# Performance work log

Hardware: AMD Instinct MI355X
Metric: run time of the kernel (lower is better)

Reference implementation:

```python
import jax, jax.numpy as jnp
import numpy as np

B, S, D, H = 2, 2048, 1024, 16
HD = D // H  # 64


def setup_inputs() -> dict:
    key = jax.random.key(0)
    ks = jax.random.split(key, 7)
    scale = 1.0 / np.sqrt(D)
    return {
        "embeddings": jax.random.normal(ks[0], (B, S, D), dtype=jnp.float32),
        "W_kv": jax.random.uniform(ks[1], (D, 2 * D), jnp.float32, -scale, scale),
        "b_kv": jax.random.uniform(ks[2], (2 * D,), jnp.float32, -scale, scale),
        "W_q": jax.random.uniform(ks[3], (D, D), jnp.float32, -scale, scale),
        "b_q": jax.random.uniform(ks[4], (D,), jnp.float32, -scale, scale),
        "W_o": jax.random.uniform(ks[5], (D, D), jnp.float32, -scale, scale),
        "b_o": jax.random.uniform(ks[6], (D,), jnp.float32, -scale, scale),
    }


def reference(embeddings, W_kv, b_kv, W_q, b_q, W_o, b_o):
    # kv projection -> [B, S, H, 2*HD] -> [B, H, S, 2*HD]
    kv = (embeddings @ W_kv + b_kv).reshape(B, S, H, 2 * HD).transpose(0, 2, 1, 3)
    q = (embeddings @ W_q + b_q).reshape(B, S, H, HD).transpose(0, 2, 1, 3)
    k, v = kv[..., :HD], kv[..., HD:]
    # naive scaled dot-product attention (full [B,H,S,S] score matrix)
    scores = jnp.einsum("bhqd,bhkd->bhqk", q, k) / jnp.sqrt(jnp.float32(HD))
    attn = jax.nn.softmax(scores, axis=-1)
    ctx = jnp.einsum("bhqk,bhkd->bhqd", attn, v)  # [B,H,S,HD]
    ctx = ctx.transpose(0, 2, 1, 3).reshape(B, S, D)
    return ctx @ W_o + b_o
```

## Files before the change

### kernel.cpp

```cpp
#include <hip/hip_runtime.h>
#include <hip/hip_bf16.h>


typedef unsigned short ushort;
typedef __attribute__((ext_vector_type(4))) float f32x4;
typedef __attribute__((ext_vector_type(16))) float f32x16;
typedef __attribute__((ext_vector_type(8))) __bf16 bf16x8;
typedef __attribute__((ext_vector_type(8))) unsigned short u16x8;
typedef __attribute__((ext_vector_type(4))) unsigned short u16x4;
typedef __attribute__((ext_vector_type(4))) unsigned int u32x4;

#define LOG2E 1.44269504088896340736f

constexpr int Bc = 2, Sc = 2048, Dc = 1024, Hc = 16, HDc = 64;

__device__ inline ushort f2bf(float f) {
    unsigned u = __builtin_bit_cast(unsigned, f);
    u += 0x7fffu + ((u >> 16) & 1u);
    return (ushort)(u >> 16);
}

__device__ inline float fexp2(float x) {
#if __has_builtin(__builtin_amdgcn_exp2f)
    return __builtin_amdgcn_exp2f(x);
#else
    return exp2f(x);
#endif
}

__device__ inline void gload16(const void* g, void* l) {
    __builtin_amdgcn_global_load_lds((const __attribute__((address_space(1))) void*)g,
                                     (__attribute__((address_space(3))) void*)l, 16, 0, 0);
}

__device__ inline f32x4 mfma16(bf16x8 a, bf16x8 b, f32x4 c) {
    return __builtin_amdgcn_mfma_f32_16x16x32_bf16(a, b, c, 0, 0, 0);
}
__device__ inline f32x16 mfma32(bf16x8 a, bf16x8 b, f32x16 c) {
    return __builtin_amdgcn_mfma_f32_32x32x16_bf16(a, b, c, 0, 0, 0);
}
__device__ inline unsigned cvtpk(float lo, float hi_) {
    unsigned r; asm("v_cvt_pk_bf16_f32 %0, %1, %2" : "=v"(r) : "v"(lo), "v"(hi_)); return r;
}
__device__ inline void swap32(unsigned& a, unsigned& b) {
    asm("v_permlane32_swap_b32 %0, %1" : "+v"(a), "+v"(b));
}

__global__ __launch_bounds__(256) void prep_k(const float* __restrict__ emb,
                                              ushort* __restrict__ embb,
                                              const float* __restrict__ Wkv,
                                              const float* __restrict__ Wq,
                                              const float* __restrict__ Wo,
                                              ushort* __restrict__ WtAll) {
    const int bid = blockIdx.x;
    if (bid < 2048) {
        int i = bid * 256 + threadIdx.x;
        const float4* p = (const float4*)emb;
        float4 a = p[2 * i], b = p[2 * i + 1];
        u16x8 r;
        r[0] = f2bf(a.x); r[1] = f2bf(a.y); r[2] = f2bf(a.z); r[3] = f2bf(a.w);
        r[4] = f2bf(b.x); r[5] = f2bf(b.y); r[6] = f2bf(b.z); r[7] = f2bf(b.w);
        ((u16x8*)embb)[i] = r;
        return;
    }
    __shared__ float t[32][33];
    int tb = bid - 2048;
    const float* W; int N, rowofs;
    if (tb < 2048)      { W = Wkv; N = 2048; rowofs = 0; }
    else if (tb < 3072) { W = Wq;  N = 1024; rowofs = 2048; tb -= 2048; }
    else                { W = Wo;  N = 1024; rowofs = 3072; tb -= 3072; }
    const int nbx = N >> 5;
    const int bx = tb % nbx, by = tb / nbx;
    const int tx = threadIdx.x & 31, ty = threadIdx.x >> 5;
    const int bj = bx * 32, bi = by * 32;
#pragma unroll
    for (int i = 0; i < 4; i++) {
        int r = ty + i * 8;
        t[r][tx] = W[(size_t)(bi + r) * N + bj + tx];
    }
    __syncthreads();
#pragma unroll
    for (int i = 0; i < 4; i++) {
        int r = ty + i * 8;
        WtAll[(size_t)(rowofs + bj + r) * 1024 + bi + tx] = f2bf(t[tx][r]);
    }
}

template <int MODE>
__global__ __launch_bounds__(256) void gemm_bt_k(const ushort* __restrict__ A,
                                                 const ushort* __restrict__ Bt,
                                                 const float* __restrict__ bias,
                                                 const float* __restrict__ bias2,
                                                 void* __restrict__ Cout,
                                                 ushort* __restrict__ Vout,
                                                 ushort* __restrict__ Qout,
                                                 int M, int N, int K) {
    __shared__ __align__(16) char sA[2][8192];
    __shared__ __align__(16) char sB[2][8192];
    const int tid = threadIdx.x;
    const int nbc = N >> 7;
    const int cpx = (gridDim.x >> 3);
    const int swzb = (blockIdx.x & 7) * cpx + (blockIdx.x >> 3);
    const int brow = swzb / nbc, bcol = swzb % nbc;
    const int w = tid >> 6, lane = tid & 63;
    const int wr = w >> 1, wc = w & 1;
    const int lg = lane >> 4, l16 = lane & 15;

    f32x4 acc[4][4] = {};

    const int r0 = tid >> 2;
    const int sl = (tid & 3) ^ (r0 & 3);
    const ushort* a0 = A + (size_t)(brow * 128 + r0) * K + sl * 8;
    const ushort* a1 = A + (size_t)(brow * 128 + 64 + r0) * K + sl * 8;
    const ushort* b0 = Bt + (size_t)(bcol * 128 + r0) * K + sl * 8;
    const ushort* b1 = Bt + (size_t)(bcol * 128 + 64 + r0) * K + sl * 8;

    const int arow = wr * 64 + l16;
    const int bcolr = wc * 64 + l16;

    auto STAGE = [&](int buf, int k0) {
        gload16(a0 + k0, sA[buf] + w * 1024);
        gload16(a1 + k0, sA[buf] + 4096 + w * 1024);
        gload16(b0 + k0, sB[buf] + w * 1024);
        gload16(b1 + k0, sB[buf] + 4096 + w * 1024);
    };

    const int nk = K >> 5;
    STAGE(0, 0);

    for (int k0 = 0; k0 < nk; k0++) {
        const int buf = k0 & 1;
        if (k0 < nk - 1) {
            STAGE(buf ^ 1, (k0 + 1) << 5);
            asm volatile("s_waitcnt vmcnt(4)" ::: "memory");
        } else {
            asm volatile("s_waitcnt vmcnt(0)" ::: "memory");
        }
        __builtin_amdgcn_s_barrier();
        __builtin_amdgcn_sched_barrier(0);

        bf16x8 af[4], bfr[4];
#pragma unroll
        for (int rf = 0; rf < 4; rf++) {
            int rr = arow + rf * 16;
            af[rf] = *(const bf16x8*)(sA[buf] + rr * 64 + ((lg * 16) ^ ((rr & 3) << 4)));
        }
#pragma unroll
        for (int cf = 0; cf < 4; cf++) {
            int rr = bcolr + cf * 16;
            bfr[cf] = *(const bf16x8*)(sB[buf] + rr * 64 + ((lg * 16) ^ ((rr & 3) << 4)));
        }
#pragma unroll
        for (int rf = 0; rf < 4; rf++)
#pragma unroll
            for (int cf = 0; cf < 4; cf++)
                acc[rf][cf] = mfma16(af[rf], bfr[cf], acc[rf][cf]);
        __builtin_amdgcn_s_barrier();
    }

#pragma unroll
    for (int cf = 0; cf < 4; cf++) {
        const int col = bcol * 128 + wc * 64 + cf * 16 + l16;
        if constexpr (MODE == 3) {
            if (col < 2048) {
                const float bv = bias[col];
                const int h = col >> 7, lo = col & 127;
#pragma unroll
                for (int rf = 0; rf < 4; rf++) {
                    int row = brow * 128 + wr * 64 + rf * 16 + lg * 4;
                    int b = row >> 11, s = row & 2047;
                    if (lo < 64) {
                        ushort* Kout = (ushort*)Cout;
#pragma unroll
                        for (int r = 0; r < 4; r++)
                            Kout[((size_t)(b * 16 + h) * 2048 + s + r) * 64 + lo] =
                                f2bf(acc[rf][cf][r] + bv);
                    } else {
                        u16x4 pk;
#pragma unroll
                        for (int r = 0; r < 4; r++) pk[r] = f2bf(acc[rf][cf][r] + bv);
                        *(u16x4*)(Vout + ((size_t)(b * 16 + h) * 64 + (lo - 64)) * 2048 + s) = pk;
                    }
                }
            } else {
                const int qc = col - 2048;
                const float bv = bias2[qc];
                const float qs = 0.125f * LOG2E;
#pragma unroll
                for (int rf = 0; rf < 4; rf++) {
                    int row = brow * 128 + wr * 64 + rf * 16 + lg * 4;
#pragma unroll
                    for (int r = 0; r < 4; r++)
                        Qout[(size_t)(row + r) * 1024 + qc] =
                            f2bf((acc[rf][cf][r] + bv) * qs);
                }
            }
        } else {
            const float bv = bias[col];
#pragma unroll
            for (int rf = 0; rf < 4; rf++) {
                int row = brow * 128 + wr * 64 + rf * 16 + lg * 4;
#pragma unroll
                for (int r = 0; r < 4; r++) {
                    float v = acc[rf][cf][r] + bv;
                    if (MODE == 1) ((float*)Cout)[(size_t)(row + r) * N + col] = v;
                    else           ((ushort*)Cout)[(size_t)(row + r) * N + col] = f2bf(v);
                }
            }
        }
    }
}

__global__ __launch_bounds__(256, 2) void attn3_k(const ushort* __restrict__ Qg,
                                                  const ushort* __restrict__ Kg,
                                                  const ushort* __restrict__ Vg,
                                                  ushort* __restrict__ ctx) {
    __shared__ __align__(16) char sK[2][16384];
    __shared__ __align__(16) char sV[2][16384];
    __shared__ float lx2[256];
    const int tid = threadIdx.x;
    const int wg = ((blockIdx.x & 7) << 6) | (blockIdx.x >> 3);
    const int bh = wg >> 4, qt = wg & 15;
    const int b = bh >> 4, h = bh & 15;
    const int w = tid >> 6, lane = tid & 63;
    const int ql = lane & 31, hi = lane >> 5;
    const int ksub = w & 1;
    const int qq = w >> 1;

    const ushort* Kh = Kg + (size_t)bh * (Sc * 64);
    const ushort* Vh = Vg + (size_t)bh * (64 * Sc);

    const int qrow0 = qt * 128 + qq * 64 + ql;
    bf16x8 qf[2][4];
#pragma unroll
    for (int qg = 0; qg < 2; qg++) {
        const ushort* qp = Qg + ((size_t)(b * Sc + qrow0 + qg * 32)) * Dc + h * HDc + hi * 8;
#pragma unroll
        for (int jd = 0; jd < 4; jd++) qf[qg][jd] = *(const bf16x8*)(qp + jd * 16);
    }

    const u16x8 ones_u = {0x3F80, 0x3F80, 0x3F80, 0x3F80, 0x3F80, 0x3F80, 0x3F80, 0x3F80};
    const bf16x8 ones8 = __builtin_bit_cast(bf16x8, ones_u);

    const int l8 = lane >> 3;
    const int sl = (lane & 7) ^ l8;

    f32x16 o[2][2] = {};
    f32x16 ls[2] = {};
    const float MH = 8.0f * LOG2E;
    const int sw = (ql & 7) << 4;

    auto STAGE = [&](int buf, int kt) {
#pragma unroll
        for (int j = 0; j < 4; j++) {
            gload16(Kh + (size_t)(kt * 128 + w * 32 + j * 8 + l8) * 64 + sl * 8,
                    sK[buf] + w * 4096 + j * 1024);
            gload16(Vh + (size_t)((w & 1) * 32 + j * 8 + l8) * Sc +
                        kt * 128 + (w >> 1) * 64 + sl * 8,
                    sV[buf] + (w >> 1) * 8192 + (w & 1) * 4096 + j * 1024);
        }
    };

    int cur = 0;
    STAGE(0, 0);

    constexpr int NT = Sc / 128;
    for (int kt = 0; kt < NT; kt++) {
        if (kt < NT - 1) {
            STAGE(cur ^ 1, kt + 1);
            asm volatile("s_waitcnt vmcnt(8)" ::: "memory");
        } else {
            asm volatile("s_waitcnt vmcnt(0)" ::: "memory");
        }
        __builtin_amdgcn_s_barrier();
        __builtin_amdgcn_sched_barrier(0);

#pragma unroll
        for (int kh = 0; kh < 2; kh++) {
            bf16x8 kf[4];
            {
                const char* kb = sK[cur] + (kh * 64 + ksub * 32 + ql) * 128;
#pragma unroll
                for (int jd = 0; jd < 4; jd++)
                    kf[jd] = *(const bf16x8*)(kb + ((jd * 32 + hi * 16) ^ sw));
            }

            f32x16 st[2];
#pragma unroll
            for (int qg = 0; qg < 2; qg++)
#pragma unroll
                for (int i = 0; i < 16; i++) st[qg][i] = -MH;
            __builtin_amdgcn_s_setprio(1);
#pragma unroll
            for (int qg = 0; qg < 2; qg++)
#pragma unroll
                for (int jd = 0; jd < 4; jd++)
                    st[qg] = mfma32(kf[jd], qf[qg][jd], st[qg]);
            __builtin_amdgcn_s_setprio(0);

#pragma unroll
            for (int qg = 0; qg < 2; qg++)
#pragma unroll
                for (int i = 0; i < 16; i++) st[qg][i] = fexp2(st[qg][i]);

            bf16x8 pf[2][2];
#pragma unroll
            for (int qg = 0; qg < 2; qg++) {
                unsigned a0 = cvtpk(st[qg][0],  st[qg][1]);
                unsigned a1 = cvtpk(st[qg][2],  st[qg][3]);
                unsigned a2 = cvtpk(st[qg][4],  st[qg][5]);
                unsigned a3 = cvtpk(st[qg][6],  st[qg][7]);
                swap32(a0, a2); swap32(a1, a3);
                u32x4 f0v = {a0, a1, a2, a3};
                pf[qg][0] = __builtin_bit_cast(bf16x8, f0v);
                unsigned c0 = cvtpk(st[qg][8],  st[qg][9]);
                unsigned c1 = cvtpk(st[qg][10], st[qg][11]);
                unsigned c2 = cvtpk(st[qg][12], st[qg][13]);
                unsigned c3 = cvtpk(st[qg][14], st[qg][15]);
                swap32(c0, c2); swap32(c1, c3);
                u32x4 f1v = {c0, c1, c2, c3};
                pf[qg][1] = __builtin_bit_cast(bf16x8, f1v);
            }

            bf16x8 vf[2][2];
#pragma unroll
            for (int dg = 0; dg < 2; dg++) {
                const char* vb = sV[cur] + kh * 8192 + (dg * 32 + ql) * 128;
#pragma unroll
                for (int ks = 0; ks < 2; ks++)
                    vf[dg][ks] = *(const bf16x8*)(vb + ((ksub * 64 + ks * 32 + hi * 16) ^ sw));
            }

            __builtin_amdgcn_s_setprio(1);
#pragma unroll
            for (int qg = 0; qg < 2; qg++)
#pragma unroll
                for (int ks = 0; ks < 2; ks++) {
                    o[0][qg] = mfma32(vf[0][ks], pf[qg][ks], o[0][qg]);
                    o[1][qg] = mfma32(vf[1][ks], pf[qg][ks], o[1][qg]);
                    ls[qg]   = mfma32(ones8,     pf[qg][ks], ls[qg]);
                }
            __builtin_amdgcn_s_setprio(0);
        }

        __builtin_amdgcn_s_barrier();
        cur ^= 1;
    }

    __syncthreads();
    float* ox = qq ? (float*)sV : (float*)sK;
    if (ksub) {
#pragma unroll
        for (int dg = 0; dg < 2; dg++)
#pragma unroll
            for (int qg = 0; qg < 2; qg++)
#pragma unroll
                for (int i = 0; i < 16; i++)
                    ox[((dg * 2 + qg) * 16 + i) * 64 + lane] = o[dg][qg][i];
        lx2[(qq * 2 + 0) * 64 + lane] = ls[0][0];
        lx2[(qq * 2 + 1) * 64 + lane] = ls[1][0];
    }
    __syncthreads();
    if (!ksub) {
#pragma unroll
        for (int dg = 0; dg < 2; dg++)
#pragma unroll
            for (int qg = 0; qg < 2; qg++)
#pragma unroll
                for (int i = 0; i < 16; i++)
                    o[dg][qg][i] += ox[((dg * 2 + qg) * 16 + i) * 64 + lane];
        const float inv0 = 1.0f / (ls[0][0] + lx2[(qq * 2 + 0) * 64 + lane]);
        const float inv1 = 1.0f / (ls[1][0] + lx2[(qq * 2 + 1) * 64 + lane]);
#pragma unroll
        for (int qg = 0; qg < 2; qg++) {
            const float inv = qg ? inv1 : inv0;
            ushort* cp = ctx + ((size_t)(b * Sc + qrow0 + qg * 32)) * Dc + h * HDc;
#pragma unroll
            for (int dg = 0; dg < 2; dg++)
#pragma unroll
                for (int g = 0; g < 4; g++) {
                    u16x4 pk;
#pragma unroll
                    for (int r = 0; r < 4; r++)
                        pk[r] = f2bf(o[dg][qg][g * 4 + r] * inv);
                    *(u16x4*)(cp + dg * 32 + g * 8 + hi * 4) = pk;
                }
        }
    }
}

extern "C" void kernel_launch(void* const* d_in, const int* in_sizes, int n_in,
                              void* d_out, int out_size, void* d_ws, size_t ws_size,
                              hipStream_t stream) {
    const float* emb  = (const float*)d_in[0];
    const float* W_kv = (const float*)d_in[1];
    const float* b_kv = (const float*)d_in[2];
    const float* W_q  = (const float*)d_in[3];
    const float* b_q  = (const float*)d_in[4];
    const float* W_o  = (const float*)d_in[5];
    const float* b_o  = (const float*)d_in[6];
    float* out = (float*)d_out;

    const int BS = Bc * Sc;
    ushort* embb  = (ushort*)d_ws;
    ushort* wallt = embb  + (size_t)BS * Dc;
    ushort* wot   = wallt + (size_t)3 * Dc * Dc;
    ushort* Kb    = wallt + (size_t)4 * Dc * Dc;
    ushort* Vtb   = Kb    + (size_t)32 * Sc * HDc;
    ushort* Qb    = Vtb   + (size_t)32 * Sc * HDc;
    ushort* ctxb  = Qb    + (size_t)BS * Dc;

    prep_k<<<6144, 256, 0, stream>>>(emb, embb, W_kv, W_q, W_o, wallt);

    gemm_bt_k<3><<<(BS / 128) * (3072 / 128), 256, 0, stream>>>(
        embb, wallt, b_kv, b_q, Kb, Vtb, Qb, BS, 3072, Dc);

    attn3_k<<<Bc * Hc * (Sc / 128), 256, 0, stream>>>(Qb, Kb, Vtb, ctxb);

    gemm_bt_k<1><<<(BS / 128) * (Dc / 128), 256, 0, stream>>>(
        ctxb, wot, b_o, nullptr, out, nullptr, nullptr, BS, Dc, Dc);
}
```

Before: 113.6 us.

## Split attention keys across four waves with private LDS tiles, drop barriers

The attention kernel now processes 64 query rows per block instead of 128, and all four waves share those queries while each handles its own 32-key slice of every 128-key tile. Each wave stages its own K/V slice into a private double-buffered LDS region, so the per-tile workgroup barriers are removed and waves only wait on their own loads. Partial outputs and row sums from three waves are reduced through LDS into wave 0 at the end, and the grid doubles to 1024 blocks. In exchange, each block reloads the full K/V for half as many queries, doubling global K/V traffic, and the final cross-wave reduction is larger.

```diff
diff --git a/kernel.cpp b/kernel.cpp
--- a/kernel.cpp
+++ b/kernel.cpp
@@ -211,58 +211,56 @@
     }
 }
 
-__global__ __launch_bounds__(256, 2) void attn3_k(const ushort* __restrict__ Qg,
+__global__ __launch_bounds__(256, 2) void attn4_k(const ushort* __restrict__ Qg,
                                                   const ushort* __restrict__ Kg,
                                                   const ushort* __restrict__ Vg,
                                                   ushort* __restrict__ ctx) {
-    __shared__ __align__(16) char sK[2][16384];
-    __shared__ __align__(16) char sV[2][16384];
-    __shared__ float lx2[256];
+    __shared__ __align__(16) char sS[4][2][8192];
+    __shared__ float lxa[3 * 128];
     const int tid = threadIdx.x;
-    const int wg = ((blockIdx.x & 7) << 6) | (blockIdx.x >> 3);
-    const int bh = wg >> 4, qt = wg & 15;
+    const int wg = ((blockIdx.x & 7) << 7) | (blockIdx.x >> 3);
+    const int bh = wg >> 5, qt = wg & 31;
     const int b = bh >> 4, h = bh & 15;
     const int w = tid >> 6, lane = tid & 63;
     const int ql = lane & 31, hi = lane >> 5;
-    const int ksub = w & 1;
-    const int qq = w >> 1;
 
     const ushort* Kh = Kg + (size_t)bh * (Sc * 64);
     const ushort* Vh = Vg + (size_t)bh * (64 * Sc);
 
-    const int qrow0 = qt * 128 + qq * 64 + ql;
+    const int l8 = lane >> 3;
+    const int kch = (lane & 7) ^ l8;
+    const int vhalf = (lane & 7) >> 2;
+    const int vkk = (lane & 3) ^ (l8 & 3);
+
+    auto STAGE = [&](int buf, int kt) {
+        const int kkb = kt * 128 + w * 32;
+#pragma unroll
+        for (int j = 0; j < 4; j++) {
+            gload16(Kh + (size_t)(kkb + j * 8 + l8) * 64 + kch * 8,
+                    sS[w][buf] + j * 1024);
+            gload16(Vh + (size_t)(j * 8 + l8 + vhalf * 32) * Sc + kkb + vkk * 8,
+                    sS[w][buf] + 4096 + j * 1024);
+        }
+    };
+
+    int cur = 0;
+    STAGE(0, 0);
+
+    const int q0 = qt * 64;
     bf16x8 qf[2][4];
 #pragma unroll
     for (int qg = 0; qg < 2; qg++) {
-        const ushort* qp = Qg + ((size_t)(b * Sc + qrow0 + qg * 32)) * Dc + h * HDc + hi * 8;
+        const ushort* qp = Qg + ((size_t)(b * Sc + q0 + qg * 32 + ql)) * Dc + h * HDc + hi * 8;
 #pragma unroll
         for (int jd = 0; jd < 4; jd++) qf[qg][jd] = *(const bf16x8*)(qp + jd * 16);
     }
 
     const u16x8 ones_u = {0x3F80, 0x3F80, 0x3F80, 0x3F80, 0x3F80, 0x3F80, 0x3F80, 0x3F80};
     const bf16x8 ones8 = __builtin_bit_cast(bf16x8, ones_u);
-
-    const int l8 = lane >> 3;
-    const int sl = (lane & 7) ^ l8;
 
     f32x16 o[2][2] = {};
     f32x16 ls[2] = {};
     const float MH = 8.0f * LOG2E;
-    const int sw = (ql & 7) << 4;
-
-    auto STAGE = [&](int buf, int kt) {
-#pragma unroll
-        for (int j = 0; j < 4; j++) {
-            gload16(Kh + (size_t)(kt * 128 + w * 32 + j * 8 + l8) * 64 + sl * 8,
-                    sK[buf] + w * 4096 + j * 1024);
-            gload16(Vh + (size_t)((w & 1) * 32 + j * 8 + l8) * Sc +
-                        kt * 128 + (w >> 1) * 64 + sl * 8,
-                    sV[buf] + (w >> 1) * 8192 + (w & 1) * 4096 + j * 1024);
-        }
-    };
-
-    int cur = 0;
-    STAGE(0, 0);
 
     constexpr int NT = Sc / 128;
     for (int kt = 0; kt < NT; kt++) {
@@ -272,109 +270,109 @@
         } else {
             asm volatile("s_waitcnt vmcnt(0)" ::: "memory");
         }
-        __builtin_amdgcn_s_barrier();
         __builtin_amdgcn_sched_barrier(0);
 
-#pragma unroll
-        for (int kh = 0; kh < 2; kh++) {
-            bf16x8 kf[4];
-            {
-                const char* kb = sK[cur] + (kh * 64 + ksub * 32 + ql) * 128;
-#pragma unroll
-                for (int jd = 0; jd < 4; jd++)
-                    kf[jd] = *(const bf16x8*)(kb + ((jd * 32 + hi * 16) ^ sw));
+        const char* kb = sS[w][cur];
+        const char* vb = sS[w][cur] + 4096;
+
+        bf16x8 kf[4];
+#pragma unroll
+        for (int jd = 0; jd < 4; jd++)
+            kf[jd] = *(const bf16x8*)(kb + ql * 128 + ((((jd << 1) | hi) ^ (ql & 7)) << 4));
+
+        f32x16 st[2];
+#pragma unroll
+        for (int qg = 0; qg < 2; qg++)
+#pragma unroll
+            for (int i = 0; i < 16; i++) st[qg][i] = -MH;
+        __builtin_amdgcn_s_setprio(1);
+#pragma unroll
+        for (int qg = 0; qg < 2; qg++)
+#pragma unroll
+            for (int jd = 0; jd < 4; jd++)
+                st[qg] = mfma32(kf[jd], qf[qg][jd], st[qg]);
+        __builtin_amdgcn_s_setprio(0);
+
+#pragma unroll
+        for (int qg = 0; qg < 2; qg++)
+#pragma unroll
+            for (int i = 0; i < 16; i++) st[qg][i] = fexp2(st[qg][i]);
+
+        bf16x8 pf[2][2];
+#pragma unroll
+        for (int qg = 0; qg < 2; qg++) {
+            unsigned a0 = cvtpk(st[qg][0],  st[qg][1]);
+            unsigned a1 = cvtpk(st[qg][2],  st[qg][3]);
+            unsigned a2 = cvtpk(st[qg][4],  st[qg][5]);
+            unsigned a3 = cvtpk(st[qg][6],  st[qg][7]);
+            swap32(a0, a2); swap32(a1, a3);
+            u32x4 f0v = {a0, a1, a2, a3};
+            pf[qg][0] = __builtin_bit_cast(bf16x8, f0v);
+            unsigned c0 = cvtpk(st[qg][8],  st[qg][9]);
+            unsigned c1 = cvtpk(st[qg][10], st[qg][11]);
+            unsigned c2 = cvtpk(st[qg][12], st[qg][13]);
+            unsigned c3 = cvtpk(st[qg][14], st[qg][15]);
+            swap32(c0, c2); swap32(c1, c3);
+            u32x4 f1v = {c0, c1, c2, c3};
+            pf[qg][1] = __builtin_bit_cast(bf16x8, f1v);
+        }
+
+        bf16x8 vf[2][2];
+#pragma unroll
+        for (int dg = 0; dg < 2; dg++)
+#pragma unroll
+            for (int ks = 0; ks < 2; ks++)
+                vf[dg][ks] = *(const bf16x8*)(vb + ql * 128 + dg * 64 +
+                                              ((((ks << 1) | hi) ^ (ql & 3)) << 4));
+
+        __builtin_amdgcn_s_setprio(1);
+#pragma unroll
+        for (int qg = 0; qg < 2; qg++)
+#pragma unroll
+            for (int ks = 0; ks < 2; ks++) {
+                o[0][qg] = mfma32(vf[0][ks], pf[qg][ks], o[0][qg]);
+                o[1][qg] = mfma32(vf[1][ks], pf[qg][ks], o[1][qg]);
+                ls[qg]   = mfma32(ones8,     pf[qg][ks], ls[qg]);
             }
-
-            f32x16 st[2];
+        __builtin_amdgcn_s_setprio(0);
+
+        cur ^= 1;
+    }
+
+    __syncthreads();
+    float* ox = (float*)sS;
+    if (w) {
+        const int base = (w - 1) * 4096;
+#pragma unroll
+        for (int dg = 0; dg < 2; dg++)
 #pragma unroll
             for (int qg = 0; qg < 2; qg++)
 #pragma unroll
-                for (int i = 0; i < 16; i++) st[qg][i] = -MH;
-            __builtin_amdgcn_s_setprio(1);
-#pragma unroll
-            for (int qg = 0; qg < 2; qg++)
-#pragma unroll
-                for (int jd = 0; jd < 4; jd++)
-                    st[qg] = mfma32(kf[jd], qf[qg][jd], st[qg]);
-            __builtin_amdgcn_s_setprio(0);
-
-#pragma unroll
-            for (int qg = 0; qg < 2; qg++)
-#pragma unroll
-                for (int i = 0; i < 16; i++) st[qg][i] = fexp2(st[qg][i]);
-
-            bf16x8 pf[2][2];
-#pragma unroll
-            for (int qg = 0; qg < 2; qg++) {
-                unsigned a0 = cvtpk(st[qg][0],  st[qg][1]);
-                unsigned a1 = cvtpk(st[qg][2],  st[qg][3]);
-                unsigned a2 = cvtpk(st[qg][4],  st[qg][5]);
-                unsigned a3 = cvtpk(st[qg][6],  st[qg][7]);
-                swap32(a0, a2); swap32(a1, a3);
-                u32x4 f0v = {a0, a1, a2, a3};
-                pf[qg][0] = __builtin_bit_cast(bf16x8, f0v);
-                unsigned c0 = cvtpk(st[qg][8],  st[qg][9]);
-                unsigned c1 = cvtpk(st[qg][10], st[qg][11]);
-                unsigned c2 = cvtpk(st[qg][12], st[qg][13]);
-                unsigned c3 = cvtpk(st[qg][14], st[qg][15]);
-                swap32(c0, c2); swap32(c1, c3);
-                u32x4 f1v = {c0, c1, c2, c3};
-                pf[qg][1] = __builtin_bit_cast(bf16x8, f1v);
-            }
-
-            bf16x8 vf[2][2];
-#pragma unroll
-            for (int dg = 0; dg < 2; dg++) {
-                const char* vb = sV[cur] + kh * 8192 + (dg * 32 + ql) * 128;
-#pragma unroll
-                for (int ks = 0; ks < 2; ks++)
-                    vf[dg][ks] = *(const bf16x8*)(vb + ((ksub * 64 + ks * 32 + hi * 16) ^ sw));
-            }
-
-            __builtin_amdgcn_s_setprio(1);
-#pragma unroll
-            for (int qg = 0; qg < 2; qg++)
-#pragma unroll
-                for (int ks = 0; ks < 2; ks++) {
-                    o[0][qg] = mfma32(vf[0][ks], pf[qg][ks], o[0][qg]);
-                    o[1][qg] = mfma32(vf[1][ks], pf[qg][ks], o[1][qg]);
-                    ls[qg]   = mfma32(ones8,     pf[qg][ks], ls[qg]);
-                }
-            __builtin_amdgcn_s_setprio(0);
-        }
-
-        __builtin_amdgcn_s_barrier();
-        cur ^= 1;
-    }
-
+                for (int i = 0; i < 16; i++)
+                    ox[base + ((dg * 2 + qg) * 16 + i) * 64 + lane] = o[dg][qg][i];
+        lxa[(w - 1) * 128 + 0 * 64 + lane] = ls[0][0];
+        lxa[(w - 1) * 128 + 1 * 64 + lane] = ls[1][0];
+    }
     __syncthreads();
-    float* ox = qq ? (float*)sV : (float*)sK;
-    if (ksub) {
-#pragma unroll
-        for (int dg = 0; dg < 2; dg++)
-#pragma unroll
-            for (int qg = 0; qg < 2; qg++)
-#pragma unroll
-                for (int i = 0; i < 16; i++)
-                    ox[((dg * 2 + qg) * 16 + i) * 64 + lane] = o[dg][qg][i];
-        lx2[(qq * 2 + 0) * 64 + lane] = ls[0][0];
-        lx2[(qq * 2 + 1) * 64 + lane] = ls[1][0];
-    }
-    __syncthreads();
-    if (!ksub) {
-#pragma unroll
-        for (int dg = 0; dg < 2; dg++)
-#pragma unroll
-            for (int qg = 0; qg < 2; qg++)
-#pragma unroll
-                for (int i = 0; i < 16; i++)
-                    o[dg][qg][i] += ox[((dg * 2 + qg) * 16 + i) * 64 + lane];
-        const float inv0 = 1.0f / (ls[0][0] + lx2[(qq * 2 + 0) * 64 + lane]);
-        const float inv1 = 1.0f / (ls[1][0] + lx2[(qq * 2 + 1) * 64 + lane]);
+    if (w == 0) {
+        float l_run[2] = {ls[0][0], ls[1][0]};
+#pragma unroll
+        for (int wv = 0; wv < 3; wv++) {
+            const int base = wv * 4096;
+#pragma unroll
+            for (int dg = 0; dg < 2; dg++)
+#pragma unroll
+                for (int qg = 0; qg < 2; qg++)
+#pragma unroll
+                    for (int i = 0; i < 16; i++)
+                        o[dg][qg][i] += ox[base + ((dg * 2 + qg) * 16 + i) * 64 + lane];
+            l_run[0] += lxa[wv * 128 + 0 * 64 + lane];
+            l_run[1] += lxa[wv * 128 + 1 * 64 + lane];
+        }
 #pragma unroll
         for (int qg = 0; qg < 2; qg++) {
-            const float inv = qg ? inv1 : inv0;
-            ushort* cp = ctx + ((size_t)(b * Sc + qrow0 + qg * 32)) * Dc + h * HDc;
+            const float inv = 1.0f / l_run[qg];
+            ushort* cp = ctx + ((size_t)(b * Sc + q0 + qg * 32 + ql)) * Dc + h * HDc;
 #pragma unroll
             for (int dg = 0; dg < 2; dg++)
 #pragma unroll
@@ -415,7 +413,7 @@
     gemm_bt_k<3><<<(BS / 128) * (3072 / 128), 256, 0, stream>>>(
         embb, wallt, b_kv, b_q, Kb, Vtb, Qb, BS, 3072, Dc);
 
-    attn3_k<<<Bc * Hc * (Sc / 128), 256, 0, stream>>>(Qb, Kb, Vtb, ctxb);
+    attn4_k<<<Bc * Hc * (Sc / 64), 256, 0, stream>>>(Qb, Kb, Vtb, ctxb);
 
     gemm_bt_k<1><<<(BS / 128) * (Dc / 128), 256, 0, stream>>>(
         ctxb, wot, b_o, nullptr, out, nullptr, nullptr, BS, Dc, Dc);
```

Result: slower. 119.6 us (+5.3%).

## Software-pipeline QK^T, exp, and PV across key sub-tiles in attention loop

Applied to the files above, without the earlier changes.

Restructures the inner attention loop so that the exponentiation and PV MFMAs of the previous key sub-tile are interleaved with the QK^T MFMAs of the next sub-tile. The second half's scores and V fragments are carried in registers across iterations. A zero-initialised prologue (exp2(-128) scores times zero V) and an epilogue handle the edges. This lets transcendental ALU work overlap matrix-core work, at the cost of more live registers (extra f32x16 scores and V fragments), which may lower occupancy or cause spills.

```diff
diff --git a/kernel.cpp b/kernel.cpp
--- a/kernel.cpp
+++ b/kernel.cpp
@@ -250,6 +250,52 @@
     const float MH = 8.0f * LOG2E;
     const int sw = (ql & 7) << 4;
 
+    f32x16 stp[2];
+    bf16x8 vfp[2][2];
+#pragma unroll
+    for (int qg = 0; qg < 2; qg++)
+#pragma unroll
+        for (int i = 0; i < 16; i++) stp[qg][i] = -128.0f;
+    {
+        const u16x8 z = {0, 0, 0, 0, 0, 0, 0, 0};
+#pragma unroll
+        for (int dg = 0; dg < 2; dg++)
+#pragma unroll
+            for (int ks = 0; ks < 2; ks++) vfp[dg][ks] = __builtin_bit_cast(bf16x8, z);
+    }
+
+    auto PACK = [&](f32x16 (&s)[2], bf16x8 (&p)[2][2]) {
+#pragma unroll
+        for (int qg = 0; qg < 2; qg++) {
+            unsigned a0 = cvtpk(s[qg][0],  s[qg][1]);
+            unsigned a1 = cvtpk(s[qg][2],  s[qg][3]);
+            unsigned a2 = cvtpk(s[qg][4],  s[qg][5]);
+            unsigned a3 = cvtpk(s[qg][6],  s[qg][7]);
+            swap32(a0, a2); swap32(a1, a3);
+            u32x4 f0v = {a0, a1, a2, a3};
+            p[qg][0] = __builtin_bit_cast(bf16x8, f0v);
+            unsigned c0 = cvtpk(s[qg][8],  s[qg][9]);
+            unsigned c1 = cvtpk(s[qg][10], s[qg][11]);
+            unsigned c2 = cvtpk(s[qg][12], s[qg][13]);
+            unsigned c3 = cvtpk(s[qg][14], s[qg][15]);
+            swap32(c0, c2); swap32(c1, c3);
+            u32x4 f1v = {c0, c1, c2, c3};
+            p[qg][1] = __builtin_bit_cast(bf16x8, f1v);
+        }
+    };
+    auto PV = [&](bf16x8 (&v)[2][2], bf16x8 (&p)[2][2]) {
+        __builtin_amdgcn_s_setprio(1);
+#pragma unroll
+        for (int qg = 0; qg < 2; qg++)
+#pragma unroll
+            for (int ks = 0; ks < 2; ks++) {
+                o[0][qg] = mfma32(v[0][ks], p[qg][ks], o[0][qg]);
+                o[1][qg] = mfma32(v[1][ks], p[qg][ks], o[1][qg]);
+                ls[qg]   = mfma32(ones8,    p[qg][ks], ls[qg]);
+            }
+        __builtin_amdgcn_s_setprio(0);
+    };
+
     auto STAGE = [&](int buf, int kt) {
 #pragma unroll
         for (int j = 0; j < 4; j++) {
@@ -275,76 +321,95 @@
         __builtin_amdgcn_s_barrier();
         __builtin_amdgcn_sched_barrier(0);
 
-#pragma unroll
-        for (int kh = 0; kh < 2; kh++) {
-            bf16x8 kf[4];
-            {
-                const char* kb = sK[cur] + (kh * 64 + ksub * 32 + ql) * 128;
-#pragma unroll
-                for (int jd = 0; jd < 4; jd++)
-                    kf[jd] = *(const bf16x8*)(kb + ((jd * 32 + hi * 16) ^ sw));
-            }
-
-            f32x16 st[2];
-#pragma unroll
-            for (int qg = 0; qg < 2; qg++)
-#pragma unroll
-                for (int i = 0; i < 16; i++) st[qg][i] = -MH;
-            __builtin_amdgcn_s_setprio(1);
-#pragma unroll
-            for (int qg = 0; qg < 2; qg++)
-#pragma unroll
-                for (int jd = 0; jd < 4; jd++)
-                    st[qg] = mfma32(kf[jd], qf[qg][jd], st[qg]);
-            __builtin_amdgcn_s_setprio(0);
-
-#pragma unroll
-            for (int qg = 0; qg < 2; qg++)
-#pragma unroll
-                for (int i = 0; i < 16; i++) st[qg][i] = fexp2(st[qg][i]);
-
-            bf16x8 pf[2][2];
-#pragma unroll
-            for (int qg = 0; qg < 2; qg++) {
-                unsigned a0 = cvtpk(st[qg][0],  st[qg][1]);
-                unsigned a1 = cvtpk(st[qg][2],  st[qg][3]);
-                unsigned a2 = cvtpk(st[qg][4],  st[qg][5]);
-                unsigned a3 = cvtpk(st[qg][6],  st[qg][7]);
-                swap32(a0, a2); swap32(a1, a3);
-                u32x4 f0v = {a0, a1, a2, a3};
-                pf[qg][0] = __builtin_bit_cast(bf16x8, f0v);
-                unsigned c0 = cvtpk(st[qg][8],  st[qg][9]);
-                unsigned c1 = cvtpk(st[qg][10], st[qg][11]);
-                unsigned c2 = cvtpk(st[qg][12], st[qg][13]);
-                unsigned c3 = cvtpk(st[qg][14], st[qg][15]);
-                swap32(c0, c2); swap32(c1, c3);
-                u32x4 f1v = {c0, c1, c2, c3};
-                pf[qg][1] = __builtin_bit_cast(bf16x8, f1v);
-            }
-
-            bf16x8 vf[2][2];
-#pragma unroll
-            for (int dg = 0; dg < 2; dg++) {
-                const char* vb = sV[cur] + kh * 8192 + (dg * 32 + ql) * 128;
+        const char* kb = sK[cur];
+        const char* vb = sV[cur];
+
+        bf16x8 kf[4];
+#pragma unroll
+        for (int jd = 0; jd < 4; jd++)
+            kf[jd] = *(const bf16x8*)(kb + (ksub * 32 + ql) * 128 + ((jd * 32 + hi * 16) ^ sw));
+
+#pragma unroll
+        for (int qg = 0; qg < 2; qg++)
+#pragma unroll
+            for (int i = 0; i < 16; i++) stp[qg][i] = fexp2(stp[qg][i]);
+
+        f32x16 st0[2];
+#pragma unroll
+        for (int qg = 0; qg < 2; qg++)
+#pragma unroll
+            for (int i = 0; i < 16; i++) st0[qg][i] = -MH;
+        __builtin_amdgcn_s_setprio(1);
+#pragma unroll
+        for (int qg = 0; qg < 2; qg++)
+#pragma unroll
+            for (int jd = 0; jd < 4; jd++)
+                st0[qg] = mfma32(kf[jd], qf[qg][jd], st0[qg]);
+        __builtin_amdgcn_s_setprio(0);
+
+        {
+            bf16x8 pfp[2][2];
+            PACK(stp, pfp);
+            PV(vfp, pfp);
+        }
+
+        bf16x8 kg[4];
+#pragma unroll
+        for (int jd = 0; jd < 4; jd++)
+            kg[jd] = *(const bf16x8*)(kb + (64 + ksub * 32 + ql) * 128 + ((jd * 32 + hi * 16) ^ sw));
+
+#pragma unroll
+        for (int qg = 0; qg < 2; qg++)
+#pragma unroll
+            for (int i = 0; i < 16; i++) st0[qg][i] = fexp2(st0[qg][i]);
+
+        f32x16 st1[2];
+#pragma unroll
+        for (int qg = 0; qg < 2; qg++)
+#pragma unroll
+            for (int i = 0; i < 16; i++) st1[qg][i] = -MH;
+        __builtin_amdgcn_s_setprio(1);
+#pragma unroll
+        for (int qg = 0; qg < 2; qg++)
+#pragma unroll
+            for (int jd = 0; jd < 4; jd++)
+                st1[qg] = mfma32(kg[jd], qf[qg][jd], st1[qg]);
+        __builtin_amdgcn_s_setprio(0);
+
+        {
+            bf16x8 pf0[2][2];
+            PACK(st0, pf0);
+            bf16x8 vf0[2][2];
+#pragma unroll
+            for (int dg = 0; dg < 2; dg++)
 #pragma unroll
                 for (int ks = 0; ks < 2; ks++)
-                    vf[dg][ks] = *(const bf16x8*)(vb + ((ksub * 64 + ks * 32 + hi * 16) ^ sw));
-            }
-
-            __builtin_amdgcn_s_setprio(1);
-#pragma unroll
-            for (int qg = 0; qg < 2; qg++)
-#pragma unroll
-                for (int ks = 0; ks < 2; ks++) {
-                    o[0][qg] = mfma32(vf[0][ks], pf[qg][ks], o[0][qg]);
-                    o[1][qg] = mfma32(vf[1][ks], pf[qg][ks], o[1][qg]);
-                    ls[qg]   = mfma32(ones8,     pf[qg][ks], ls[qg]);
-                }
-            __builtin_amdgcn_s_setprio(0);
-        }
+                    vf0[dg][ks] = *(const bf16x8*)(vb + (dg * 32 + ql) * 128 +
+                                                   ((ksub * 64 + ks * 32 + hi * 16) ^ sw));
+            PV(vf0, pf0);
+        }
+
+#pragma unroll
+        for (int dg = 0; dg < 2; dg++)
+#pragma unroll
+            for (int ks = 0; ks < 2; ks++)
+                vfp[dg][ks] = *(const bf16x8*)(vb + 8192 + (dg * 32 + ql) * 128 +
+                                               ((ksub * 64 + ks * 32 + hi * 16) ^ sw));
+        stp[0] = st1[0];
+        stp[1] = st1[1];
 
         __builtin_amdgcn_s_barrier();
         cur ^= 1;
+    }
+
+#pragma unroll
+    for (int qg = 0; qg < 2; qg++)
+#pragma unroll
+        for (int i = 0; i < 16; i++) stp[qg][i] = fexp2(stp[qg][i]);
+    {
+        bf16x8 pfp[2][2];
+        PACK(stp, pfp);
+        PV(vfp, pfp);
     }
 
     __syncthreads();
```

Result: slower. 170.4 us (+50.0%).
